# Optimization experiments

Hardware: AMD Instinct MI355X
Metric: run time of the kernel (lower is better)

## Reference

```python
import jax, jax.numpy as jnp
import numpy as np

B, S, D, H = 2, 2048, 1024, 16
DK = D // H
FF_HIDDEN = 2048  # FeedForward default hidden_dim (fixed, not 4*D)


def setup_inputs() -> dict:
    key = jax.random.key(0)
    ks = jax.random.split(key, 16)
    s = 0.02
    inp = {
        "query": jax.random.normal(ks[0], (B, S, D), jnp.float32),
        "key": jax.random.normal(ks[1], (B, S, D), jnp.float32),
        "value": jax.random.normal(ks[2], (B, S, D), jnp.float32),
        "Wq": jax.random.normal(ks[3], (D, D), jnp.float32) * s,
        "bq": jnp.zeros((D,), jnp.float32),
        "Wk": jax.random.normal(ks[4], (D, D), jnp.float32) * s,
        "bk": jnp.zeros((D,), jnp.float32),
        "Wv": jax.random.normal(ks[5], (D, D), jnp.float32) * s,
        "bv": jnp.zeros((D,), jnp.float32),
        "ln_g": jnp.ones((D,), jnp.float32),
        "ln_b": jnp.zeros((D,), jnp.float32),
        "W1": jax.random.normal(ks[6], (D, FF_HIDDEN), jnp.float32) * s,
        "b1": jnp.zeros((FF_HIDDEN,), jnp.float32),
        "W2": jax.random.normal(ks[7], (FF_HIDDEN, D), jnp.float32) * s,
        "b2": jnp.zeros((D,), jnp.float32),
    }
    return inp


def reference(query, key, value, Wq, bq, Wk, bk, Wv, bv, ln_g, ln_b, W1, b1, W2, b2):
    # QKV projections
    q = query @ Wq + bq  # [B,S,D]
    k = key @ Wk + bk
    v = value @ Wv + bv
    # split heads -> [B,H,S,DK]
    q = q.reshape(B, S, H, DK).transpose(0, 2, 1, 3)
    k = k.reshape(B, S, H, DK).transpose(0, 2, 1, 3)
    v = v.reshape(B, S, H, DK).transpose(0, 2, 1, 3)
    # naive attention: full [B,H,S,S] scores (faithful to source)
    scores = jnp.einsum("bhqd,bhkd->bhqk", q, k) / jnp.sqrt(jnp.float32(DK))
    probs = jax.nn.softmax(scores, axis=-1)  # dropout = identity (eval)
    attn = jnp.einsum("bhqk,bhkd->bhqd", probs, v)
    attn = attn.transpose(0, 2, 1, 3).reshape(B, S, D)
    # LayerNorm
    mu = attn.mean(axis=-1, keepdims=True)
    var = attn.var(axis=-1, keepdims=True)
    ffi = (attn - mu) / jnp.sqrt(var + 1e-5) * ln_g + ln_b
    # FeedForward (dropout = identity in eval)
    h = jax.nn.relu(ffi @ W1 + b1)
    ff = h @ W2 + b2
    return ffi + ff
```

## Files before the change

### kernel.cpp

```cpp
#include <hip/hip_runtime.h>
#include <hip/hip_bf16.h>


#define S_LEN 2048
#define DMODEL 1024
#define NROWS 4096
#define QSCALE (0.125f * 1.4426950408889634f)

typedef __attribute__((ext_vector_type(8))) short short8_t;
typedef __attribute__((ext_vector_type(4))) float f32x4;

__device__ __forceinline__ unsigned short f2bf(float f){
  union { float f; unsigned int u; } a; a.f = f;
  unsigned int r = a.u + 0x7fffu + ((a.u >> 16) & 1u);
  return (unsigned short)(r >> 16);
}
__device__ __forceinline__ unsigned int pack2(float lo, float hi){
  return (unsigned int)f2bf(lo) | ((unsigned int)f2bf(hi) << 16);
}
__device__ __forceinline__ unsigned int cvtpk(float lo, float hi){
  unsigned int r;
  asm("v_cvt_pk_bf16_f32 %0, %1, %2" : "=v"(r) : "v"(lo), "v"(hi));
  return r;
}
__device__ __forceinline__ void gload_lds16(const void* g, void* l){
  __builtin_amdgcn_global_load_lds((const __attribute__((address_space(1))) unsigned int*)g,
                                   (__attribute__((address_space(3))) unsigned int*)l, 16, 0, 0);
}

__global__ __launch_bounds__(256) void cast3_kernel(const float* __restrict__ q,
    const float* __restrict__ k, const float* __restrict__ v, unsigned short* __restrict__ out){
  const float* src = blockIdx.y == 0 ? q : (blockIdx.y == 1 ? k : v);
  size_t i = (size_t)(blockIdx.x * 256 + threadIdx.x) * 8;
  float4 a = *(const float4*)(src + i);
  float4 b = *(const float4*)(src + i + 4);
  uint4 u; u.x = pack2(a.x,a.y); u.y = pack2(a.z,a.w); u.z = pack2(b.x,b.y); u.w = pack2(b.z,b.w);
  *(uint4*)(out + (size_t)blockIdx.y*4194304 + i) = u;
}

__device__ __forceinline__ void tc_body(const float* __restrict__ in,
    unsigned short* __restrict__ out, int R, int C, int bx, int by){
  __shared__ __align__(16) unsigned short tile[64*76];
  int c0 = bx * 64, r0 = by * 64;
  int t = threadIdx.x;
#pragma unroll
  for (int i = 0; i < 4; i++){
    int slot = i*256 + t;
    int r = slot >> 4, c4 = slot & 15;
    float4 v = *(const float4*)(in + (size_t)(r0 + r)*C + c0 + c4*4);
    ushort4 u; u.x = f2bf(v.x); u.y = f2bf(v.y); u.z = f2bf(v.z); u.w = f2bf(v.w);
    *(ushort4*)&tile[r*76 + c4*4] = u;
  }
  __syncthreads();
#pragma unroll
  for (int i = 0; i < 4; i++){
    int slot = i*256 + t;
    int oc = slot >> 4, seg = slot & 15;
    ushort4 u;
    u.x = tile[(seg*4+0)*76 + oc];
    u.y = tile[(seg*4+1)*76 + oc];
    u.z = tile[(seg*4+2)*76 + oc];
    u.w = tile[(seg*4+3)*76 + oc];
    *(ushort4*)(out + (size_t)(c0 + oc)*R + r0 + seg*4) = u;
  }
}
__global__ __launch_bounds__(256) void transpose_cast_f32(const float* __restrict__ in,
    unsigned short* __restrict__ out, int R, int C){
  tc_body(in, out, R, C, blockIdx.x, blockIdx.y);
}
__global__ __launch_bounds__(256) void transpose_cast_w3(const float* __restrict__ w0,
    const float* __restrict__ w1, const float* __restrict__ w2, unsigned short* __restrict__ out){
  const float* in = blockIdx.z == 0 ? w0 : (blockIdx.z == 1 ? w1 : w2);
  tc_body(in, out + (size_t)blockIdx.z*1048576, 1024, 1024, blockIdx.x, blockIdx.y);
}

__global__ __launch_bounds__(256) void transpose_bf16(const unsigned short* __restrict__ in,
    unsigned short* __restrict__ out, int R, int C, int inStride){
  __shared__ __align__(16) unsigned short tile[64*76];
  int c0 = blockIdx.x * 64, r0 = blockIdx.y * 64;
  int t = threadIdx.x;
#pragma unroll
  for (int i = 0; i < 2; i++){
    int slot = i*256 + t;
    int r = slot >> 3, c8 = slot & 7;
    uint4 v = *(const uint4*)(in + (size_t)(r0 + r)*inStride + c0 + c8*8);
    uint2 lo; lo.x = v.x; lo.y = v.y;
    uint2 hi; hi.x = v.z; hi.y = v.w;
    *(uint2*)&tile[r*76 + c8*8]     = lo;
    *(uint2*)&tile[r*76 + c8*8 + 4] = hi;
  }
  __syncthreads();
#pragma unroll
  for (int i = 0; i < 4; i++){
    int slot = i*256 + t;
    int oc = slot >> 4, seg = slot & 15;
    ushort4 u;
    u.x = tile[(seg*4+0)*76 + oc];
    u.y = tile[(seg*4+1)*76 + oc];
    u.z = tile[(seg*4+2)*76 + oc];
    u.w = tile[(seg*4+3)*76 + oc];
    *(ushort4*)(out + (size_t)(c0 + oc)*R + r0 + seg*4) = u;
  }
}

__global__ __launch_bounds__(256) void concat_bias(const float* __restrict__ a,
    const float* __restrict__ b, const float* __restrict__ c, float* __restrict__ o){
  int i = blockIdx.x*256 + threadIdx.x;
  o[i] = i < 1024 ? a[i] : (i < 2048 ? b[i-1024] : c[i-2048]);
}

template<bool OBF16, bool RELU, bool RESID, int NF>
__global__ __launch_bounds__(256, 2) void gemm_bt(
    const unsigned short* __restrict__ A, const unsigned short* __restrict__ Bt,
    const float* __restrict__ bias, float scale, int scale_ncols, size_t aSel,
    unsigned short* __restrict__ Ob, float* __restrict__ Of,
    const float* __restrict__ resid, int M, int N, int K)
{
  __shared__ __align__(16) unsigned short As[2*128*64];
  __shared__ __align__(16) unsigned short Bs[2*32*NF*64];
  char* AsB = (char*)As;
  char* BsB = (char*)Bs;
  int tid = threadIdx.x, lane = tid & 63, wave = tid >> 6;
  int wr = wave >> 1, wc = wave & 1;
  int m0 = blockIdx.y * 128, n0 = blockIdx.x * (32*NF);
  int qr = lane & 15, g = lane >> 4;
  f32x4 acc[4][NF];
#pragma unroll
  for (int i = 0; i < 4; i++)
#pragma unroll
    for (int j = 0; j < NF; j++) acc[i][j] = (f32x4){0.f,0.f,0.f,0.f};

  int lr = lane >> 3, ls = lane & 7;
  int scol = (ls ^ lr) * 8;
  const unsigned short* Ag = A + (size_t)(n0 >> 10)*aSel + (size_t)(m0 + wave*32 + lr)*K + scol;
  const unsigned short* Bg = Bt + (size_t)(n0 + wave*8*NF + lr)*K + scol;

  int rx = qr & 7;
  int aoff = (wr*64 + qr)*128 + ((g ^ rx) << 4);
  int boff = (wc*16*NF + qr)*128 + ((g ^ rx) << 4);

  int NT = K >> 6;
#pragma unroll
  for (int i = 0; i < 4; i++)
    gload_lds16(Ag + (size_t)i*8*K, AsB + wave*4096 + i*1024);
#pragma unroll
  for (int i = 0; i < NF; i++)
    gload_lds16(Bg + (size_t)i*8*K, BsB + wave*NF*1024 + i*1024);

  for (int it = 0; it < NT; ++it){
    int cur = it & 1;
    if (it + 1 < NT){
      int k1 = (it + 1) << 6;
      char* ad = AsB + (cur^1)*16384 + wave*4096;
      char* bd = BsB + (cur^1)*NF*4096 + wave*NF*1024;
#pragma unroll
      for (int i = 0; i < 4; i++)
        gload_lds16(Ag + (size_t)i*8*K + k1, ad + i*1024);
#pragma unroll
      for (int i = 0; i < NF; i++)
        gload_lds16(Bg + (size_t)i*8*K + k1, bd + i*1024);
      if constexpr (NF == 4) asm volatile("s_waitcnt vmcnt(8)" ::: "memory");
      else                   asm volatile("s_waitcnt vmcnt(6)" ::: "memory");
    } else {
      asm volatile("s_waitcnt vmcnt(0)" ::: "memory");
    }
    __builtin_amdgcn_s_barrier();
    asm volatile("" ::: "memory");

    const char* ka = AsB + cur*16384;
    const char* kb = BsB + cur*NF*4096;
    short8_t af[2][4], bfv[2][NF];
#pragma unroll
    for (int mi = 0; mi < 4; mi++){
      af[0][mi] = *(const short8_t*)(ka + aoff + mi*2048);
      af[1][mi] = *(const short8_t*)(ka + (aoff^64) + mi*2048);
    }
#pragma unroll
    for (int ni = 0; ni < NF; ni++){
      bfv[0][ni] = *(const short8_t*)(kb + boff + ni*2048);
      bfv[1][ni] = *(const short8_t*)(kb + (boff^64) + ni*2048);
    }
#pragma unroll
    for (int kh = 0; kh < 2; kh++)
#pragma unroll
      for (int mi = 0; mi < 4; mi++)
#pragma unroll
        for (int ni = 0; ni < NF; ni++)
          acc[mi][ni] = __builtin_amdgcn_mfma_f32_16x16x32_bf16(af[kh][mi], bfv[kh][ni], acc[mi][ni], 0, 0, 0);

    asm volatile("s_waitcnt lgkmcnt(0)" ::: "memory");
    __builtin_amdgcn_s_barrier();
    asm volatile("" ::: "memory");
  }
#pragma unroll
  for (int ni = 0; ni < NF; ni++){
    int col = n0 + wc*16*NF + ni*16 + qr;
    float bs = bias[col];
    float sc = (col < scale_ncols) ? scale : 1.f;
#pragma unroll
    for (int mi = 0; mi < 4; mi++){
#pragma unroll
      for (int r = 0; r < 4; r++){
        int row = m0 + wr*64 + mi*16 + g*4 + r;
        float v = (acc[mi][ni][r] + bs) * sc;
        if constexpr (RELU) v = fmaxf(v, 0.f);
        if constexpr (RESID) v += resid[(size_t)row*N + col];
        if constexpr (OBF16) Ob[(size_t)row*N + col] = f2bf(v);
        else                 Of[(size_t)row*N + col] = v;
      }
    }
  }
}

__global__ __launch_bounds__(256, 4) void flash_attn(
    const unsigned short* __restrict__ qkv,
    const unsigned short* __restrict__ vT,
    float* __restrict__ attn)
{
  __shared__ __align__(16) char smem[40960];
  int tid = threadIdx.x, lane = tid & 63, wave = tid >> 6;
  int bid = blockIdx.x;
  int orig = (bid & 7) * 128 + (bid >> 3);
  int bh = orig >> 5, qb = orig & 31;
  int b = bh >> 4, h = bh & 15;
  int q0 = qb * 64 + wave * 16;
  int qr = lane & 15, g = lane >> 4;

  const unsigned short* qptr = qkv + (size_t)(b*S_LEN + q0 + qr)*3072 + h*64 + g*8;
  short8_t qf0 = *(const short8_t*)qptr;
  short8_t qf1 = *(const short8_t*)(qptr + 32);

  const f32x4 z4 = {0.f,0.f,0.f,0.f};
  f32x4 oacc[4];
#pragma unroll
  for (int tv = 0; tv < 4; tv++) oacc[tv] = z4;
  float lsum = 0.f;

  int lrow = lane >> 3, lslot = lane & 7;
  int sw = (lslot ^ lrow) * 8;
  const unsigned short* kg = qkv + 1024 + (size_t)(b*S_LEN + wave*8 + lrow)*3072 + h*64 + sw;
  const unsigned short* vg = vT + (size_t)(h*64 + wave*8 + lrow)*4096 + b*S_LEN + sw;

  int rx = qr & 7;
  int koff0 = qr*128 + ((g ^ rx) * 16);
  int koff1 = koff0 ^ 64;

  char* Pb = smem + 32768 + wave*2048;
  int gh = g >> 1;
  int pw0 = qr*128 + 8*(g & 1);
  int pr0 = qr*128;

  {
    char* kb_ = smem + wave*1024;
    char* vb_ = smem + 16384 + wave*1024;
    gload_lds16(kg,                       kb_);
    gload_lds16(kg + (size_t)32*3072,     kb_ + 4096);
    gload_lds16(vg,                       vb_);
    gload_lds16(vg + (size_t)32*4096,     vb_ + 4096);
  }

  int cur = 0;
  for (int it = 0; it < S_LEN/64; ++it){
    if (it + 1 < S_LEN/64){
      int kv1 = (it + 1) * 64;
      char* kb_ = smem + (cur^1)*8192 + wave*1024;
      char* vb_ = smem + 16384 + (cur^1)*8192 + wave*1024;
      gload_lds16(kg + (size_t)kv1*3072,        kb_);
      gload_lds16(kg + (size_t)(kv1+32)*3072,   kb_ + 4096);
      gload_lds16(vg + kv1,                     vb_);
      gload_lds16(vg + (size_t)32*4096 + kv1,   vb_ + 4096);
      asm volatile("s_waitcnt vmcnt(4)" ::: "memory");
    } else {
      asm volatile("s_waitcnt vmcnt(0)" ::: "memory");
    }
    __builtin_amdgcn_s_barrier();
    asm volatile("" ::: "memory");

    const char* kb = smem + cur*8192;
    const char* vb = smem + 16384 + cur*8192;

    f32x4 st[4];
    __builtin_amdgcn_s_setprio(1);
#pragma unroll
    for (int t = 0; t < 4; t++){
      short8_t kf0 = *(const short8_t*)(kb + koff0 + t*2048);
      short8_t kf1 = *(const short8_t*)(kb + koff1 + t*2048);
      st[t] = __builtin_amdgcn_mfma_f32_16x16x32_bf16(kf0, qf0, z4, 0, 0, 0);
      st[t] = __builtin_amdgcn_mfma_f32_16x16x32_bf16(kf1, qf1, st[t], 0, 0, 0);
    }
    __builtin_amdgcn_s_setprio(0);

    float ps0 = 0.f, ps1 = 0.f;
#pragma unroll
    for (int t = 0; t < 4; t++){
      float p0 = exp2f(st[t][0]);
      float p1 = exp2f(st[t][1]);
      float p2 = exp2f(st[t][2]);
      float p3 = exp2f(st[t][3]);
      uint2 wv; wv.x = cvtpk(p0, p1); wv.y = cvtpk(p2, p3);
      *(uint2*)(Pb + pw0 + (((2*t + gh) ^ rx) << 4)) = wv;
      ps0 += p0 + p1;
      ps1 += p2 + p3;
    }
    lsum += ps0 + ps1;

    short8_t pf0 = *(const short8_t*)(Pb + pr0 + (((0 + g) ^ rx) << 4));
    short8_t pf1 = *(const short8_t*)(Pb + pr0 + (((4 + g) ^ rx) << 4));

    __builtin_amdgcn_s_setprio(1);
#pragma unroll
    for (int tv = 0; tv < 4; tv++){
      short8_t vf0 = *(const short8_t*)(vb + koff0 + tv*2048);
      short8_t vf1 = *(const short8_t*)(vb + koff1 + tv*2048);
      oacc[tv] = __builtin_amdgcn_mfma_f32_16x16x32_bf16(vf0, pf0, oacc[tv], 0, 0, 0);
      oacc[tv] = __builtin_amdgcn_mfma_f32_16x16x32_bf16(vf1, pf1, oacc[tv], 0, 0, 0);
    }
    __builtin_amdgcn_s_setprio(0);

    asm volatile("s_waitcnt lgkmcnt(0)" ::: "memory");
    __builtin_amdgcn_s_barrier();
    asm volatile("" ::: "memory");
    cur ^= 1;
  }
  lsum += __shfl_xor(lsum, 16, 64);
  lsum += __shfl_xor(lsum, 32, 64);
  float inv = 1.f / lsum;

  __syncthreads();
  float* ot = (float*)(smem + wave*4160);
#pragma unroll
  for (int tv = 0; tv < 4; tv++)
#pragma unroll
    for (int r = 0; r < 4; r++)
      ot[qr*65 + tv*16 + g*4 + r] = oacc[tv][r] * inv;
  __syncthreads();
  int row = lane >> 2, seg = lane & 3;
  const float* src = ot + row*65 + seg*16;
  float* dst = attn + (size_t)(b*S_LEN + qb*64 + wave*16 + row)*DMODEL + h*64 + seg*16;
#pragma unroll
  for (int i = 0; i < 4; i++){
    float4 v; v.x = src[i*4]; v.y = src[i*4+1]; v.z = src[i*4+2]; v.w = src[i*4+3];
    *(float4*)(dst + i*4) = v;
  }
}

__global__ __launch_bounds__(256) void layernorm_kernel(const float* __restrict__ x,
    const float* __restrict__ gw, const float* __restrict__ bw,
    float* __restrict__ y, unsigned short* __restrict__ yb)
{
  int row = blockIdx.x, t = threadIdx.x;
  float4 v = *(const float4*)(x + (size_t)row*DMODEL + t*4);
  float s = (v.x + v.y) + (v.z + v.w);
  float q = (v.x*v.x + v.y*v.y) + (v.z*v.z + v.w*v.w);
#pragma unroll
  for (int off = 1; off < 64; off <<= 1){
    s += __shfl_xor(s, off, 64);
    q += __shfl_xor(q, off, 64);
  }
  __shared__ float red[8];
  if ((t & 63) == 0){ red[(t >> 6)*2] = s; red[(t >> 6)*2 + 1] = q; }
  __syncthreads();
  s = red[0] + red[2] + red[4] + red[6];
  q = red[1] + red[3] + red[5] + red[7];
  float mu = s * (1.f/DMODEL);
  float var = q * (1.f/DMODEL) - mu*mu;
  float rstd = rsqrtf(var + 1e-5f);
  float4 gg = *(const float4*)(gw + t*4);
  float4 bb = *(const float4*)(bw + t*4);
  float4 o;
  o.x = (v.x - mu)*rstd*gg.x + bb.x;
  o.y = (v.y - mu)*rstd*gg.y + bb.y;
  o.z = (v.z - mu)*rstd*gg.z + bb.z;
  o.w = (v.w - mu)*rstd*gg.w + bb.w;
  *(float4*)(y + (size_t)row*DMODEL + t*4) = o;
  uint2 u; u.x = pack2(o.x, o.y); u.y = pack2(o.z, o.w);
  *(uint2*)(yb + (size_t)row*DMODEL + t*4) = u;
}

extern "C" void kernel_launch(void* const* d_in, const int* in_sizes, int n_in,
                              void* d_out, int out_size, void* d_ws, size_t ws_size,
                              hipStream_t stream)
{
  const float* query = (const float*)d_in[0];
  const float* key_  = (const float*)d_in[1];
  const float* value = (const float*)d_in[2];
  const float* Wq = (const float*)d_in[3];
  const float* bq = (const float*)d_in[4];
  const float* Wk = (const float*)d_in[5];
  const float* bk = (const float*)d_in[6];
  const float* Wv = (const float*)d_in[7];
  const float* bv = (const float*)d_in[8];
  const float* ln_g = (const float*)d_in[9];
  const float* ln_b = (const float*)d_in[10];
  const float* W1 = (const float*)d_in[11];
  const float* b1 = (const float*)d_in[12];
  const float* W2 = (const float*)d_in[13];
  const float* b2 = (const float*)d_in[14];

  char* ws = (char*)d_ws;
  unsigned short* qx     = (unsigned short*)(ws + 0);
  unsigned short* WqkvT  = (unsigned short*)(ws + 25165824);
  unsigned short* W1T    = (unsigned short*)(ws + 31457280);
  unsigned short* W2T    = (unsigned short*)(ws + 35651584);
  unsigned short* qkvbuf = (unsigned short*)(ws + 39845888);
  unsigned short* vTb    = (unsigned short*)(ws + 65011712);
  float*          attnf  = (float*)(ws + 73400320);
  unsigned short* hbuf   = (unsigned short*)(ws + 73400320);
  float*          biascat= (float*)(ws + 73400320 + 8388608);
  float*          ffif   = (float*)(ws + 90177536);
  unsigned short* ffib   = (unsigned short*)(ws + 106954752);

  cast3_kernel<<<dim3(2048,3), 256, 0, stream>>>(query, key_, value, qx);
  transpose_cast_w3<<<dim3(16,16,3), 256, 0, stream>>>(Wq, Wk, Wv, WqkvT);
  transpose_cast_f32<<<dim3(32,16), 256, 0, stream>>>(W1, W1T, 1024, 2048);
  transpose_cast_f32<<<dim3(16,32), 256, 0, stream>>>(W2, W2T, 2048, 1024);
  concat_bias<<<12, 256, 0, stream>>>(bq, bk, bv, biascat);

  gemm_bt<true,false,false,4><<<dim3(24,32), 256, 0, stream>>>(
      qx, WqkvT, biascat, QSCALE, 1024, (size_t)4194304, qkvbuf, nullptr, nullptr, 4096, 3072, 1024);
  transpose_bf16<<<dim3(16,64), 256, 0, stream>>>(qkvbuf + 2048, vTb, 4096, 1024, 3072);
  flash_attn<<<1024, 256, 0, stream>>>(qkvbuf, vTb, attnf);
  layernorm_kernel<<<4096, 256, 0, stream>>>(attnf, ln_g, ln_b, ffif, ffib);
  gemm_bt<true,true,false,4><<<dim3(16,32), 256, 0, stream>>>(
      ffib, W1T, b1, 1.f, 0, (size_t)0, hbuf, nullptr, nullptr, 4096, 2048, 1024);
  gemm_bt<false,false,true,2><<<dim3(16,32), 256, 0, stream>>>(
      hbuf, W2T, b2, 1.f, 0, (size_t)0, nullptr, (float*)d_out, ffif, 4096, 1024, 2048);
}
```

Before: 199.8 us.

## Process two 16-row query groups per wave in flash attention

Each wave now handles 32 query rows instead of 16, so every K and V tile staged in LDS is reused for twice as many MFMAs. The grid halves to 512 blocks of 128 queries, the P scratch and output staging buffers double, and launch bounds drop to two blocks per SM. This cuts K/V global-to-LDS traffic and LDS reads per unit of compute, at the cost of more registers, more shared memory and lower occupancy.

```diff
diff --git a/kernel.cpp b/kernel.cpp
--- a/kernel.cpp
+++ b/kernel.cpp
@@ -212,40 +212,46 @@
   }
 }
 
-__global__ __launch_bounds__(256, 4) void flash_attn(
+__global__ __launch_bounds__(256, 2) void flash_attn(
     const unsigned short* __restrict__ qkv,
     const unsigned short* __restrict__ vT,
     float* __restrict__ attn)
 {
-  __shared__ __align__(16) char smem[40960];
+  __shared__ __align__(16) char smem[49152];
   int tid = threadIdx.x, lane = tid & 63, wave = tid >> 6;
   int bid = blockIdx.x;
-  int orig = (bid & 7) * 128 + (bid >> 3);
-  int bh = orig >> 5, qb = orig & 31;
-  int b = bh >> 4, h = bh & 15;
-  int q0 = qb * 64 + wave * 16;
+  int orig = (bid & 7) * 64 + (bid >> 3);
+  int bh = orig >> 4, qb = orig & 15;
+  int b = bh >> 4, hd = bh & 15;
+  int q0 = qb * 128 + wave * 32;
   int qr = lane & 15, g = lane >> 4;
 
-  const unsigned short* qptr = qkv + (size_t)(b*S_LEN + q0 + qr)*3072 + h*64 + g*8;
-  short8_t qf0 = *(const short8_t*)qptr;
-  short8_t qf1 = *(const short8_t*)(qptr + 32);
+  short8_t qf[2][2];
+#pragma unroll
+  for (int qg = 0; qg < 2; qg++){
+    const unsigned short* qptr = qkv + (size_t)(b*S_LEN + q0 + 16*qg + qr)*3072 + hd*64 + g*8;
+    qf[qg][0] = *(const short8_t*)qptr;
+    qf[qg][1] = *(const short8_t*)(qptr + 32);
+  }
 
   const f32x4 z4 = {0.f,0.f,0.f,0.f};
-  f32x4 oacc[4];
-#pragma unroll
-  for (int tv = 0; tv < 4; tv++) oacc[tv] = z4;
-  float lsum = 0.f;
+  f32x4 oacc[4][2];
+#pragma unroll
+  for (int tv = 0; tv < 4; tv++)
+#pragma unroll
+    for (int qg = 0; qg < 2; qg++) oacc[tv][qg] = z4;
+  float lsum[2] = {0.f, 0.f};
 
   int lrow = lane >> 3, lslot = lane & 7;
   int sw = (lslot ^ lrow) * 8;
-  const unsigned short* kg = qkv + 1024 + (size_t)(b*S_LEN + wave*8 + lrow)*3072 + h*64 + sw;
-  const unsigned short* vg = vT + (size_t)(h*64 + wave*8 + lrow)*4096 + b*S_LEN + sw;
+  const unsigned short* kg = qkv + 1024 + (size_t)(b*S_LEN + wave*8 + lrow)*3072 + hd*64 + sw;
+  const unsigned short* vg = vT + (size_t)(hd*64 + wave*8 + lrow)*4096 + b*S_LEN + sw;
 
   int rx = qr & 7;
   int koff0 = qr*128 + ((g ^ rx) * 16);
   int koff1 = koff0 ^ 64;
 
-  char* Pb = smem + 32768 + wave*2048;
+  char* Pb = smem + 32768 + wave*4096;
   int gh = g >> 1;
   int pw0 = qr*128 + 8*(g & 1);
   int pr0 = qr*128;
@@ -279,41 +285,54 @@
     const char* kb = smem + cur*8192;
     const char* vb = smem + 16384 + cur*8192;
 
-    f32x4 st[4];
+    f32x4 st[4][2];
     __builtin_amdgcn_s_setprio(1);
 #pragma unroll
     for (int t = 0; t < 4; t++){
       short8_t kf0 = *(const short8_t*)(kb + koff0 + t*2048);
       short8_t kf1 = *(const short8_t*)(kb + koff1 + t*2048);
-      st[t] = __builtin_amdgcn_mfma_f32_16x16x32_bf16(kf0, qf0, z4, 0, 0, 0);
-      st[t] = __builtin_amdgcn_mfma_f32_16x16x32_bf16(kf1, qf1, st[t], 0, 0, 0);
+#pragma unroll
+      for (int qg = 0; qg < 2; qg++){
+        st[t][qg] = __builtin_amdgcn_mfma_f32_16x16x32_bf16(kf0, qf[qg][0], z4, 0, 0, 0);
+        st[t][qg] = __builtin_amdgcn_mfma_f32_16x16x32_bf16(kf1, qf[qg][1], st[t][qg], 0, 0, 0);
+      }
     }
     __builtin_amdgcn_s_setprio(0);
 
-    float ps0 = 0.f, ps1 = 0.f;
-#pragma unroll
-    for (int t = 0; t < 4; t++){
-      float p0 = exp2f(st[t][0]);
-      float p1 = exp2f(st[t][1]);
-      float p2 = exp2f(st[t][2]);
-      float p3 = exp2f(st[t][3]);
-      uint2 wv; wv.x = cvtpk(p0, p1); wv.y = cvtpk(p2, p3);
-      *(uint2*)(Pb + pw0 + (((2*t + gh) ^ rx) << 4)) = wv;
-      ps0 += p0 + p1;
-      ps1 += p2 + p3;
-    }
-    lsum += ps0 + ps1;
-
-    short8_t pf0 = *(const short8_t*)(Pb + pr0 + (((0 + g) ^ rx) << 4));
-    short8_t pf1 = *(const short8_t*)(Pb + pr0 + (((4 + g) ^ rx) << 4));
+#pragma unroll
+    for (int qg = 0; qg < 2; qg++){
+      float ps0 = 0.f, ps1 = 0.f;
+#pragma unroll
+      for (int t = 0; t < 4; t++){
+        float p0 = exp2f(st[t][qg][0]);
+        float p1 = exp2f(st[t][qg][1]);
+        float p2 = exp2f(st[t][qg][2]);
+        float p3 = exp2f(st[t][qg][3]);
+        uint2 wv; wv.x = cvtpk(p0, p1); wv.y = cvtpk(p2, p3);
+        *(uint2*)(Pb + qg*2048 + pw0 + (((2*t + gh) ^ rx) << 4)) = wv;
+        ps0 += p0 + p1;
+        ps1 += p2 + p3;
+      }
+      lsum[qg] += ps0 + ps1;
+    }
+
+    short8_t pf[2][2];
+#pragma unroll
+    for (int qg = 0; qg < 2; qg++){
+      pf[0][qg] = *(const short8_t*)(Pb + qg*2048 + pr0 + (((0 + g) ^ rx) << 4));
+      pf[1][qg] = *(const short8_t*)(Pb + qg*2048 + pr0 + (((4 + g) ^ rx) << 4));
+    }
 
     __builtin_amdgcn_s_setprio(1);
 #pragma unroll
     for (int tv = 0; tv < 4; tv++){
       short8_t vf0 = *(const short8_t*)(vb + koff0 + tv*2048);
       short8_t vf1 = *(const short8_t*)(vb + koff1 + tv*2048);
-      oacc[tv] = __builtin_amdgcn_mfma_f32_16x16x32_bf16(vf0, pf0, oacc[tv], 0, 0, 0);
-      oacc[tv] = __builtin_amdgcn_mfma_f32_16x16x32_bf16(vf1, pf1, oacc[tv], 0, 0, 0);
+#pragma unroll
+      for (int qg = 0; qg < 2; qg++){
+        oacc[tv][qg] = __builtin_amdgcn_mfma_f32_16x16x32_bf16(vf0, pf[0][qg], oacc[tv][qg], 0, 0, 0);
+        oacc[tv][qg] = __builtin_amdgcn_mfma_f32_16x16x32_bf16(vf1, pf[1][qg], oacc[tv][qg], 0, 0, 0);
+      }
     }
     __builtin_amdgcn_s_setprio(0);
 
@@ -322,25 +341,36 @@
     asm volatile("" ::: "memory");
     cur ^= 1;
   }
-  lsum += __shfl_xor(lsum, 16, 64);
-  lsum += __shfl_xor(lsum, 32, 64);
-  float inv = 1.f / lsum;
+  float inv[2];
+#pragma unroll
+  for (int qg = 0; qg < 2; qg++){
+    float l = lsum[qg];
+    l += __shfl_xor(l, 16, 64);
+    l += __shfl_xor(l, 32, 64);
+    inv[qg] = 1.f / l;
+  }
 
   __syncthreads();
-  float* ot = (float*)(smem + wave*4160);
-#pragma unroll
-  for (int tv = 0; tv < 4; tv++)
-#pragma unroll
-    for (int r = 0; r < 4; r++)
-      ot[qr*65 + tv*16 + g*4 + r] = oacc[tv][r] * inv;
+  float* ot = (float*)(smem + wave*8320);
+#pragma unroll
+  for (int qg = 0; qg < 2; qg++)
+#pragma unroll
+    for (int tv = 0; tv < 4; tv++)
+#pragma unroll
+      for (int r = 0; r < 4; r++)
+        ot[(qg*16 + qr)*65 + tv*16 + g*4 + r] = oacc[tv][qg][r] * inv[qg];
   __syncthreads();
-  int row = lane >> 2, seg = lane & 3;
-  const float* src = ot + row*65 + seg*16;
-  float* dst = attn + (size_t)(b*S_LEN + qb*64 + wave*16 + row)*DMODEL + h*64 + seg*16;
-#pragma unroll
-  for (int i = 0; i < 4; i++){
-    float4 v; v.x = src[i*4]; v.y = src[i*4+1]; v.z = src[i*4+2]; v.w = src[i*4+3];
-    *(float4*)(dst + i*4) = v;
+  int seg = lane & 3;
+#pragma unroll
+  for (int rr = 0; rr < 2; rr++){
+    int row = rr*16 + (lane >> 2);
+    const float* src = ot + row*65 + seg*16;
+    float* dst = attn + (size_t)(b*S_LEN + qb*128 + wave*32 + row)*DMODEL + hd*64 + seg*16;
+#pragma unroll
+    for (int i = 0; i < 4; i++){
+      float4 v; v.x = src[i*4]; v.y = src[i*4+1]; v.z = src[i*4+2]; v.w = src[i*4+3];
+      *(float4*)(dst + i*4) = v;
+    }
   }
 }
 
@@ -419,7 +449,7 @@
   gemm_bt<true,false,false,4><<<dim3(24,32), 256, 0, stream>>>(
       qx, WqkvT, biascat, QSCALE, 1024, (size_t)4194304, qkvbuf, nullptr, nullptr, 4096, 3072, 1024);
   transpose_bf16<<<dim3(16,64), 256, 0, stream>>>(qkvbuf + 2048, vTb, 4096, 1024, 3072);
-  flash_attn<<<1024, 256, 0, stream>>>(qkvbuf, vTb, attnf);
+  flash_attn<<<512, 256, 0, stream>>>(qkvbuf, vTb, attnf);
   layernorm_kernel<<<4096, 256, 0, stream>>>(attnf, ln_g, ln_b, ffif, ffib);
   gemm_bt<true,true,false,4><<<dim3(16,32), 256, 0, stream>>>(
       ffib, W1T, b1, 1.f, 0, (size_t)0, hbuf, nullptr, nullptr, 4096, 2048, 1024);
```

Measured after the change: 197.8 us. No clear change (-1.0%).
